# Kernel optimization log

Hardware: AMD Instinct MI355X
Metric: run time of the kernel (lower is better)

The kernel has to match this reference:

```python
import jax, jax.numpy as jnp
import numpy as np
import math

D, H = 128, 8
B, LC, LQ = 8, 512, 64


def pos_signal(channels, length):
    # tensor2tensor timing signal, returned as [C, L]
    pos = jnp.arange(length, dtype=jnp.float32)
    nts = channels // 2
    inc = math.log(1.0e4) / (nts - 1)
    inv = jnp.exp(jnp.arange(nts, dtype=jnp.float32) * -inc)
    st = pos[:, None] * inv[None, :]                      # [L, nts]
    sig = jnp.concatenate([jnp.sin(st), jnp.cos(st)], 1)  # [L, C]
    return sig.T


def mask_logits(t, m):
    return t * m + (1.0 - m) * -1e30


def ln_c(x, g, b):  # LayerNorm over channel dim of [B, D, L]
    mu = jnp.mean(x, axis=1, keepdims=True)
    var = jnp.mean((x - mu) ** 2, axis=1, keepdims=True)
    return (x - mu) / jnp.sqrt(var + 1e-5) * g[None, :, None] + b[None, :, None]


def conv1x1(x, w, b=None):  # x [B, I, L], w [O, I]
    y = jnp.einsum('oi,bil->bol', w, x)
    return y if b is None else y + b[None, :, None]


def dw_sep_conv(x, dw, pw, pwb):  # depthwise (k, no bias) -> pointwise (bias) -> relu
    k = dw.shape[-1]
    y = jax.lax.conv_general_dilated(x, dw[:, None, :], (1,), [(k // 2, k // 2)],
        dimension_numbers=('NCH', 'OIH', 'NCH'), feature_group_count=x.shape[1])
    return jax.nn.relu(conv1x1(y, pw, pwb))


def self_attention(x, mem_w, q_w, mask, n_head):  # x [B, D, L]
    b, d, L = x.shape
    dh = d // n_head
    mem = jnp.einsum('oi,bil->blo', mem_w, x)  # [B, L, 2D]
    q = jnp.einsum('oi,bil->blo', q_w, x)      # [B, L, D]
    def heads(t):
        return t.reshape(b, L, n_head, dh).transpose(0, 2, 1, 3)  # [B, H, L, dh]
    Qh = heads(q) * dh ** -0.5
    K = heads(mem[..., :d])
    V = heads(mem[..., d:])
    logits = jnp.einsum('bhqe,bhke->bhqk', Qh, K)
    logits = mask_logits(logits, mask[:, None, None, :])
    w = jax.nn.softmax(logits, axis=-1)
    o = jnp.einsum('bhqk,bhke->bhqe', w, V)
    return o.transpose(0, 2, 1, 3).reshape(b, L, d).transpose(0, 2, 1)


def encoder_block(x, mask, p, n_head):
    out = x + pos_signal(x.shape[1], x.shape[2])[None]
    n_conv = p['dw'].shape[0]
    for i in range(n_conv):
        res = out
        out = ln_c(out, p['lnc_g'][i], p['lnc_b'][i])
        out = dw_sep_conv(out, p['dw'][i], p['pw'][i], p['pw_b'][i]) + res
    res = out
    out = ln_c(out, p['ln1_g'], p['ln1_b'])
    out = self_attention(out, p['mem_w'], p['q_w'], mask, n_head) + res
    res = out
    out = ln_c(out, p['ln2_g'], p['ln2_b'])
    out = jax.nn.relu(conv1x1(out, p['ffn1_w'], p['ffn1_b']))
    out = conv1x1(out, p['ffn2_w'], p['ffn2_b'])
    return out + res


def cq_attention(Ce, Qe, cmask, qmask, w4C, w4Q, w4mlu, cq_b):
    Cx = Ce.transpose(0, 2, 1)   # [B, Lc, 2D]
    Qx = Qe.transpose(0, 2, 1)   # [B, Lq, 2D]
    s0 = jnp.einsum('bld,d->bl', Cx, w4C)[:, :, None]
    s1 = jnp.einsum('bqd,d->bq', Qx, w4Q)[:, None, :]
    s2 = jnp.einsum('bld,bqd->blq', Cx * w4mlu[None, None, :], Qx)
    S = s0 + s1 + s2 + cq_b
    S1 = jax.nn.softmax(mask_logits(S, qmask[:, None, :]), axis=2)
    S2 = jax.nn.softmax(mask_logits(S, cmask[:, :, None]), axis=1)
    A = jnp.einsum('blq,bqd->bld', S1, Qx)
    Bt = jnp.einsum('blq,bmq,bmd->bld', S1, S2, Cx)  # (S1 @ S2^T) @ C
    out = jnp.concatenate([Cx, A, Cx * A, Cx * Bt], axis=2)
    return out.transpose(0, 2, 1)  # [B, 8D, Lc]


def _forward(C, Q, maskC, maskQ, e_dw, e_pw, e_pw_b, e_lnc_g, e_lnc_b, e_mem_w, e_q_w,
             e_ffn1_w, e_ffn1_b, e_ffn2_w, e_ffn2_b, e_ln1_g, e_ln1_b, e_ln2_g, e_ln2_b,
             w4C, w4Q, w4mlu, cq_b, resizer_w,
             m_dw, m_pw, m_pw_b, m_lnc_g, m_lnc_b, m_mem_w, m_q_w,
             m_ffn1_w, m_ffn1_b, m_ffn2_w, m_ffn2_b, m_ln1_g, m_ln1_b, m_ln2_g, m_ln2_b):
    ep = dict(dw=e_dw, pw=e_pw, pw_b=e_pw_b, lnc_g=e_lnc_g, lnc_b=e_lnc_b,
              mem_w=e_mem_w, q_w=e_q_w, ffn1_w=e_ffn1_w, ffn1_b=e_ffn1_b,
              ffn2_w=e_ffn2_w, ffn2_b=e_ffn2_b, ln1_g=e_ln1_g, ln1_b=e_ln1_b,
              ln2_g=e_ln2_g, ln2_b=e_ln2_b)
    mp = dict(dw=m_dw, pw=m_pw, pw_b=m_pw_b, lnc_g=m_lnc_g, lnc_b=m_lnc_b,
              mem_w=m_mem_w, q_w=m_q_w, ffn1_w=m_ffn1_w, ffn1_b=m_ffn1_b,
              ffn2_w=m_ffn2_w, ffn2_b=m_ffn2_b, ln1_g=m_ln1_g, ln1_b=m_ln1_b,
              ln2_g=m_ln2_g, ln2_b=m_ln2_b)
    Ce = encoder_block(C, maskC, ep, H)
    Qe = encoder_block(Q, maskQ, ep, H)
    Ce = jnp.concatenate([Ce, C], axis=1)  # encode_fusion -> [B, 2D, Lc]
    Qe = jnp.concatenate([Qe, Q], axis=1)
    X = cq_attention(Ce, Qe, maskC, maskQ, w4C, w4Q, w4mlu, cq_b)
    X = jnp.concatenate([X, Ce], axis=1)   # match_fusion -> [B, 10D, Lc]
    M0 = conv1x1(X, resizer_w)             # [B, D, Lc]

    def run(m):
        def step(carry, p):
            return encoder_block(carry, maskC, p, H), None
        m, _ = jax.lax.scan(step, m, mp)
        return m

    M1 = run(M0)
    M2 = run(M1)
    M3 = run(M2)
    return M1, M2, M3


def setup_inputs() -> dict:
    key = jax.random.key(0)
    ks = iter(jax.random.split(key, 48))
    def rn(shape, scale):
        return jax.random.normal(next(ks), shape, dtype=jnp.float32) * scale
    s1 = 1.0 / math.sqrt(D)
    s2 = 1.0 / math.sqrt(2 * D)
    f32 = jnp.float32
    return dict(
        C=rn((B, D, LC), 1.0), Q=rn((B, D, LQ), 1.0),
        maskC=jnp.ones((B, LC), f32), maskQ=jnp.ones((B, LQ), f32),
        e_dw=rn((4, D, 7), 1.0 / math.sqrt(7)), e_pw=rn((4, D, D), s1),
        e_pw_b=jnp.zeros((4, D), f32), e_lnc_g=jnp.ones((4, D), f32), e_lnc_b=jnp.zeros((4, D), f32),
        e_mem_w=rn((2 * D, D), s1), e_q_w=rn((D, D), s1),
        e_ffn1_w=rn((D, D), s1), e_ffn1_b=jnp.zeros((D,), f32),
        e_ffn2_w=rn((D, D), s1), e_ffn2_b=jnp.zeros((D,), f32),
        e_ln1_g=jnp.ones((D,), f32), e_ln1_b=jnp.zeros((D,), f32),
        e_ln2_g=jnp.ones((D,), f32), e_ln2_b=jnp.zeros((D,), f32),
        w4C=rn((2 * D,), s2), w4Q=rn((2 * D,), s2), w4mlu=rn((2 * D,), s2),
        cq_b=jnp.zeros((1,), f32),
        resizer_w=rn((D, 10 * D), 1.0 / math.sqrt(10 * D)),
        m_dw=rn((7, 2, D, 5), 1.0 / math.sqrt(5)), m_pw=rn((7, 2, D, D), s1),
        m_pw_b=jnp.zeros((7, 2, D), f32), m_lnc_g=jnp.ones((7, 2, D), f32), m_lnc_b=jnp.zeros((7, 2, D), f32),
        m_mem_w=rn((7, 2 * D, D), s1), m_q_w=rn((7, D, D), s1),
        m_ffn1_w=rn((7, D, D), s1), m_ffn1_b=jnp.zeros((7, D), f32),
        m_ffn2_w=rn((7, D, D), s1), m_ffn2_b=jnp.zeros((7, D), f32),
        m_ln1_g=jnp.ones((7, D), f32), m_ln1_b=jnp.zeros((7, D), f32),
        m_ln2_g=jnp.ones((7, D), f32), m_ln2_b=jnp.zeros((7, D), f32),
    )


def reference(C, Q, maskC, maskQ, e_dw, e_pw, e_pw_b, e_lnc_g, e_lnc_b, e_mem_w, e_q_w,
              e_ffn1_w, e_ffn1_b, e_ffn2_w, e_ffn2_b, e_ln1_g, e_ln1_b, e_ln2_g, e_ln2_b,
              w4C, w4Q, w4mlu, cq_b, resizer_w,
              m_dw, m_pw, m_pw_b, m_lnc_g, m_lnc_b, m_mem_w, m_q_w,
              m_ffn1_w, m_ffn1_b, m_ffn2_w, m_ffn2_b, m_ln1_g, m_ln1_b, m_ln2_g, m_ln2_b):
    return _forward(C, Q, maskC, maskQ, e_dw, e_pw, e_pw_b, e_lnc_g, e_lnc_b, e_mem_w, e_q_w,
                    e_ffn1_w, e_ffn1_b, e_ffn2_w, e_ffn2_b, e_ln1_g, e_ln1_b, e_ln2_g, e_ln2_b,
                    w4C, w4Q, w4mlu, cq_b, resizer_w,
                    m_dw, m_pw, m_pw_b, m_lnc_g, m_lnc_b, m_mem_w, m_q_w,
                    m_ffn1_w, m_ffn1_b, m_ffn2_w, m_ffn2_b, m_ln1_g, m_ln1_b, m_ln2_g, m_ln2_b)
```

## Files before the change

kernel.cpp:

```cpp
#include <hip/hip_runtime.h>
#include <math.h>

#define D_  128
#define B_  8
#define H_  8
#define LC_ 512
#define LQ_ 64

typedef float f32x4 __attribute__((ext_vector_type(4)));
typedef short bf16x8 __attribute__((ext_vector_type(8)));
typedef short short4v __attribute__((ext_vector_type(4)));
typedef unsigned short ushortT;

__device__ inline short bfr(float x) {
  unsigned u = __float_as_uint(x);
  u += 0x7fff + ((u >> 16) & 1);
  return (short)(u >> 16);
}
__device__ inline float bfi(ushortT u) {
  return __uint_as_float(((unsigned)u) << 16);
}

__device__ inline bf16x8 mk8(short4v lo, short4v hi) {
  bf16x8 r;
  r[0] = lo[0]; r[1] = lo[1]; r[2] = lo[2]; r[3] = lo[3];
  r[4] = hi[0]; r[5] = hi[1]; r[6] = hi[2]; r[7] = hi[3];
  return r;
}

__device__ inline bf16x8 ldA(const ushortT* row, int koff) {
  short4v lo = *(const short4v*)(row + koff);
  short4v hi = *(const short4v*)(row + koff + 16);
  return mk8(lo, hi);
}
__device__ inline bf16x8 ldB2(const ushortT* plo, const ushortT* phi) {
  short4v lo = *(const short4v*)plo;
  short4v hi = *(const short4v*)phi;
  return mk8(lo, hi);
}

__global__ void k_prep(const float* a0, const float* a1, const float* a2,
                       const float* a3, const float* a4, const float* a5,
                       const float* a6, const float* a7, const float* a8,
                       const float* a9, const float* a10, ushortT* dst) {
  int i = blockIdx.x * 256 + threadIdx.x;
  if (i >= 1114112) return;
  const float* s; int lo;
  if      (i <   65536) { s = a0;  lo = i; }
  else if (i <   98304) { s = a1;  lo = i - 65536; }
  else if (i <  114688) { s = a2;  lo = i - 98304; }
  else if (i <  131072) { s = a3;  lo = i - 114688; }
  else if (i <  147456) { s = a4;  lo = i - 131072; }
  else if (i <  311296) { s = a5;  lo = i - 147456; }
  else if (i <  540672) { s = a6;  lo = i - 311296; }
  else if (i <  770048) { s = a7;  lo = i - 540672; }
  else if (i <  884736) { s = a8;  lo = i - 770048; }
  else if (i <  999424) { s = a9;  lo = i - 884736; }
  else                  { s = a10; lo = i - 999424; }
  dst[i] = (ushortT)bfr(s[lo]);
}

template <int KK, int ADDPOS>
__global__ __launch_bounds__(256) void k_fusedconv(
    const float* __restrict__ xC, float* __restrict__ yC,
    const float* __restrict__ xQ, float* __restrict__ yQ,
    const float* __restrict__ dw1, const ushortT* __restrict__ pw1,
    const float* __restrict__ pb1, const float* __restrict__ g1,
    const float* __restrict__ be1,
    const float* __restrict__ dw2, const ushortT* __restrict__ pw2,
    const float* __restrict__ pb2, const float* __restrict__ g2w,
    const float* __restrict__ be2, int ntC) {
  const int HALO = KK / 2;
  const int W1 = 32 + 2 * HALO;
  __shared__ __align__(16) float raw[128 * 40];
  __shared__ __align__(16) ushortT l1o[128 * 36];
  __shared__ __align__(16) ushortT xbf1[32 * 32 * 4];
  __shared__ float mu1[40], rs1[40], mu2[32], rs2[32], ps[160], psq[160];
  ushortT* xbf2 = (ushortT*)raw;
  int bx = blockIdx.x;
  const float* x; float* yout; int l0, L;
  if (bx < ntC) { x = xC; yout = yC; l0 = bx * 16; L = LC_; }
  else          { x = xQ; yout = yQ; l0 = (bx - ntC) * 16; L = LQ_; }
  int o0 = blockIdx.y * 64;
  int b = blockIdx.z;
  int tid = threadIdx.x;
  for (int idx = tid; idx < 128 * W1; idx += 256) {
    int d = idx / W1, c = idx - d * W1;
    int gl = l0 - 8 - HALO + c;
    float v = 0.f;
    if (gl >= 0 && gl < L) {
      v = x[((size_t)b * 128 + d) * L + gl];
      if (ADDPOS) {
        int j = d & 63;
        float arg = (float)gl * expf(-(float)j * 0.14619588f);
        v += (d < 64) ? sinf(arg) : cosf(arg);
      }
    }
    raw[d * 40 + c] = v;
  }
  __syncthreads();
  if (tid < 4 * W1) {
    int c = tid % W1, hh = tid / W1;
    float s = 0.f, s2 = 0.f;
    for (int d = hh * 32; d < hh * 32 + 32; d++) {
      float v = raw[d * 40 + c];
      s += v; s2 += v * v;
    }
    ps[tid] = s; psq[tid] = s2;
  }
  __syncthreads();
  if (tid < W1) {
    float s = ps[tid] + ps[tid + W1] + ps[tid + 2 * W1] + ps[tid + 3 * W1];
    float s2 = psq[tid] + psq[tid + W1] + psq[tid + 2 * W1] + psq[tid + 3 * W1];
    float mu = s * (1.f / 128.f);
    float var = fmaxf(s2 * (1.f / 128.f) - mu * mu, 0.f);
    mu1[tid] = mu; rs1[tid] = rsqrtf(var + 1e-5f);
  }
  __syncthreads();
  {
    int cc0 = tid & 31, dbase = tid >> 5;
#pragma unroll
    for (int kq = 0; kq < 4; kq++) {
      short4v pk;
#pragma unroll
      for (int e = 0; e < 4; e++) {
        int d = dbase * 16 + kq * 4 + e;
        float gg = g1[d], bb = be1[d];
        const float* wr = dw1 + d * KK;
        float acc = 0.f;
#pragma unroll
        for (int t = 0; t < KK; t++) {
          int ci = cc0 + t;
          int gl = l0 - 8 - HALO + ci;
          float lv = 0.f;
          if (gl >= 0 && gl < L)
            lv = (raw[d * 40 + ci] - mu1[ci]) * rs1[ci] * gg + bb;
          acc += wr[t] * lv;
        }
        pk[e] = bfr(acc);
      }
      *(short4v*)&xbf1[(((dbase * 4 + kq) * 32) + cc0) * 4] = pk;
    }
  }
  __syncthreads();
  int w = tid >> 6, lane = tid & 63, g2 = lane >> 4, r = lane & 15;
  {
    f32x4 acc[2][2];
#pragma unroll
    for (int i = 0; i < 2; i++)
// ... 43 lines not shown
    float s = ps[tid] + ps[tid + 32] + ps[tid + 64] + ps[tid + 96];
    float s2 = psq[tid] + psq[tid + 32] + psq[tid + 64] + psq[tid + 96];
    float mu = s * (1.f / 128.f);
    float var = fmaxf(s2 * (1.f / 128.f) - mu * mu, 0.f);
    mu2[tid] = mu; rs2[tid] = rsqrtf(var + 1e-5f);
  }
  __syncthreads();
  {
    int cc2 = tid & 15, db2 = tid >> 4;
#pragma unroll
    for (int kq = 0; kq < 2; kq++) {
      short4v pk;
#pragma unroll
      for (int e = 0; e < 4; e++) {
        int d = db2 * 8 + kq * 4 + e;
        float gg = g2w[d], bb = be2[d];
        const float* wr = dw2 + d * KK;
        float acc = 0.f;
#pragma unroll
        for (int t = 0; t < KK; t++) {
          int c1 = cc2 + 8 + t - HALO;
          int gl = l0 + cc2 + t - HALO;
          float lv = 0.f;
          if (gl >= 0 && gl < L)
            lv = (bfi(l1o[d * 36 + c1]) - mu2[c1]) * rs2[c1] * gg + bb;
          acc += wr[t] * lv;
        }
        pk[e] = bfr(acc);
      }
      *(short4v*)&xbf2[(((db2 * 2 + kq) * 16) + cc2) * 4] = pk;
    }
  }
  __syncthreads();
  {
    f32x4 a2 = {0.f, 0.f, 0.f, 0.f};
    const ushortT* arow = pw2 + (size_t)(o0 + 16 * w + r) * 128;
#pragma unroll
    for (int kk = 0; kk < 4; kk++) {
      bf16x8 a = ldA(arow, kk * 32 + g2 * 4);
      bf16x8 bb = ldB2(&xbf2[(((kk * 8 + g2) * 16) + r) * 4],
                       &xbf2[(((kk * 8 + 4 + g2) * 16) + r) * 4]);
      a2 = __builtin_amdgcn_mfma_f32_16x16x32_bf16(a, bb, a2, 0, 0, 0);
    }
#pragma unroll
    for (int p = 0; p < 4; p++) {
      int o = o0 + 16 * w + g2 * 4 + p;
      yout[((size_t)b * 128 + o) * L + l0 + r] =
          fmaxf(a2[p] + pb2[o], 0.f) + bfi(l1o[o * 36 + 8 + r]);
    }
  }
}

template <int KK, int ADDPOS>
__global__ __launch_bounds__(1024) void k_convproj1024(
    const float* __restrict__ xC, float* __restrict__ yC,
    float* __restrict__ mkvC, float* __restrict__ qpC,
    const float* __restrict__ xQ, float* __restrict__ yQ,
    float* __restrict__ mkvQ, float* __restrict__ qpQ,
    const float* __restrict__ dw1, const ushortT* __restrict__ pw1,
    const float* __restrict__ pb1, const float* __restrict__ g1,
    const float* __restrict__ be1,
    const float* __restrict__ dw2, const ushortT* __restrict__ pw2,
    const float* __restrict__ pb2, const float* __restrict__ g2w,
    const float* __restrict__ be2,
    const ushortT* __restrict__ memw, const ushortT* __restrict__ qw,
    const float* __restrict__ g3, const float* __restrict__ be3, int ntC) {
  const int HALO = KK / 2;
  const int W1 = 32 + 2 * HALO;
  __shared__ __align__(16) float raw[128 * 40];
  __shared__ __align__(16) ushortT l1o[128 * 36];
  __shared__ __align__(16) ushortT xbf1[32 * 32 * 4];
  __shared__ __align__(16) ushortT c2o[128 * 16];
  __shared__ float mu1[40], rs1[40], mu2[32], rs2[32], mu3[16], rs3[16];
  __shared__ float ps[160], psq[160];
  ushortT* xbf2 = (ushortT*)raw;
  ushortT* xbf3 = (ushortT*)(raw + 4096);
  int bx = blockIdx.x;
  const float* x; float* yout; float* mkv; float* qp; int l0, L;
  if (bx < ntC) { x = xC; yout = yC; mkv = mkvC; qp = qpC; l0 = bx * 16; L = LC_; }
  else          { x = xQ; yout = yQ; mkv = mkvQ; qp = qpQ; l0 = (bx - ntC) * 16; L = LQ_; }
  int b = blockIdx.z;
  int tid = threadIdx.x;
  for (int idx = tid; idx < 128 * W1; idx += 1024) {
    int d = idx / W1, c = idx - d * W1;
    int gl = l0 - 8 - HALO + c;
    float v = 0.f;
    if (gl >= 0 && gl < L) {
      v = x[((size_t)b * 128 + d) * L + gl];
      if (ADDPOS) {
        int j = d & 63;
        float arg = (float)gl * expf(-(float)j * 0.14619588f);
        v += (d < 64) ? sinf(arg) : cosf(arg);
      }
    }
    raw[d * 40 + c] = v;
  }
  __syncthreads();
  if (tid < 4 * W1) {
    int c = tid % W1, hh = tid / W1;
    float s = 0.f, s2 = 0.f;
    for (int d = hh * 32; d < hh * 32 + 32; d++) {
      float v = raw[d * 40 + c];
      s += v; s2 += v * v;
    }
    ps[tid] = s; psq[tid] = s2;
  }
  __syncthreads();
  if (tid < W1) {
    float s = ps[tid] + ps[tid + W1] + ps[tid + 2 * W1] + ps[tid + 3 * W1];
    float s2 = psq[tid] + psq[tid + W1] + psq[tid + 2 * W1] + psq[tid + 3 * W1];
    float mu = s * (1.f / 128.f);
    float var = fmaxf(s2 * (1.f / 128.f) - mu * mu, 0.f);
    mu1[tid] = mu; rs1[tid] = rsqrtf(var + 1e-5f);
  }
  __syncthreads();
  {
    int cc0 = tid & 31, dbase = tid >> 5;
    short4v pk;
#pragma unroll
    for (int e = 0; e < 4; e++) {
      int d = dbase * 4 + e;
      float gg = g1[d], bb = be1[d];
      const float* wr = dw1 + d * KK;
      float acc = 0.f;
#pragma unroll
      for (int t = 0; t < KK; t++) {
        int ci = cc0 + t;
        int gl = l0 - 8 - HALO + ci;
        float lv = 0.f;
        if (gl >= 0 && gl < L)
          lv = (raw[d * 40 + ci] - mu1[ci]) * rs1[ci] * gg + bb;
        acc += wr[t] * lv;
      }
      pk[e] = bfr(acc);
    }
    *(short4v*)&xbf1[((dbase * 32) + cc0) * 4] = pk;
  }
  __syncthreads();
  int w = tid >> 6, lane = tid & 63, g2 = lane >> 4, r = lane & 15;
  {
    int m = w & 7, nt = w >> 3;
    f32x4 acc = {0.f, 0.f, 0.f, 0.f};
    const ushortT* arow = pw1 + (size_t)(m * 16 + r) * 128;
#pragma unroll
    for (int kk = 0; kk < 4; kk++) {
      bf16x8 a = ldA(arow, kk * 32 + g2 * 4);
      bf16x8 bb = ldB2(&xbf1[(((kk * 8 + g2) * 32) + nt * 16 + r) * 4],
                       &xbf1[(((kk * 8 + 4 + g2) * 32) + nt * 16 + r) * 4]);
      acc = __builtin_amdgcn_mfma_f32_16x16x32_bf16(a, bb, acc, 0, 0, 0);
    }
#pragma unroll
    for (int p = 0; p < 4; p++) {
      int o = m * 16 + g2 * 4 + p;
      int c1 = nt * 16 + r;
      int gl = l0 - 8 + c1;
      float val = 0.f;
      if (gl >= 0 && gl < L)
        val = fmaxf(acc[p] + pb1[o], 0.f) + raw[o * 40 + c1 + HALO];
      l1o[o * 36 + c1] = (ushortT)bfr(val);
    }
  }
  __syncthreads();
  if (tid < 128) {
    int c = tid & 31, hh = tid >> 5;
    float s = 0.f, s2 = 0.f;
    for (int d = hh * 32; d < hh * 32 + 32; d++) {
      float v = bfi(l1o[d * 36 + c]);
      s += v; s2 += v * v;
    }
    ps[tid] = s; psq[tid] = s2;
  }
  __syncthreads();
  if (tid < 32) {
    float s = ps[tid] + ps[tid + 32] + ps[tid + 64] + ps[tid + 96];
    float s2 = psq[tid] + psq[tid + 32] + psq[tid + 64] + psq[tid + 96];
    float mu = s * (1.f / 128.f);
    float var = fmaxf(s2 * (1.f / 128.f) - mu * mu, 0.f);
    mu2[tid] = mu; rs2[tid] = rsqrtf(var + 1e-5f);
  }
  __syncthreads();
  {
    int cc2 = tid & 15, db2 = tid >> 4;
#pragma unroll
    for (int e = 0; e < 2; e++) {
      int d = db2 * 2 + e;
      float gg = g2w[d], bb = be2[d];
      const float* wr = dw2 + d * KK;
      float acc = 0.f;
#pragma unroll
      for (int t = 0; t < KK; t++) {
        int c1 = cc2 + 8 + t - HALO;
        int gl = l0 + cc2 + t - HALO;
        float lv = 0.f;
        if (gl >= 0 && gl < L)
          lv = (bfi(l1o[d * 36 + c1]) - mu2[c1]) * rs2[c1] * gg + bb;
        acc += wr[t] * lv;
      }
      xbf2[(((d >> 2) * 16) + cc2) * 4 + (d & 3)] = (ushortT)bfr(acc);
    }
  }
  __syncthreads();
  if (w < 8) {
    f32x4 a2 = {0.f, 0.f, 0.f, 0.f};
    const ushortT* arow = pw2 + (size_t)(w * 16 + r) * 128;
#pragma unroll
    for (int kk = 0; kk < 4; kk++) {
      bf16x8 a = ldA(arow, kk * 32 + g2 * 4);
      bf16x8 bb = ldB2(&xbf2[(((kk * 8 + g2) * 16) + r) * 4],
                       &xbf2[(((kk * 8 + 4 + g2) * 16) + r) * 4]);
      a2 = __builtin_amdgcn_mfma_f32_16x16x32_bf16(a, bb, a2, 0, 0, 0);
    }
#pragma unroll
    for (int p = 0; p < 4; p++) {
      int o = w * 16 + g2 * 4 + p;
      float val = fmaxf(a2[p] + pb2[o], 0.f) + bfi(l1o[o * 36 + 8 + r]);
      yout[((size_t)b * 128 + o) * L + l0 + r] = val;
      c2o[o * 16 + r] = (ushortT)bfr(val);
    }
  }
  __syncthreads();
  if (tid < 128) {
    int c = tid & 15, hh = tid >> 4;
    float s = 0.f, s2 = 0.f;
    for (int d = hh * 16; d < hh * 16 + 16; d++) {
      float v = bfi(c2o[d * 16 + c]);
      s += v; s2 += v * v;
    }
    ps[tid] = s; psq[tid] = s2;
  }
  __syncthreads();
  if (tid < 16) {
    float s = 0.f, s2 = 0.f;
#pragma unroll
    for (int hh = 0; hh < 8; hh++) { s += ps[hh * 16 + tid]; s2 += psq[hh * 16 + tid]; }
    float mu = s * (1.f / 128.f);
    float var = fmaxf(s2 * (1.f / 128.f) - mu * mu, 0.f);
    mu3[tid] = mu; rs3[tid] = rsqrtf(var + 1e-5f);
  }
  __syncthreads();
  for (int idx = tid; idx < 2048; idx += 1024) {
    int d = idx >> 4, c = idx & 15;
    float val = (bfi(c2o[d * 16 + c]) - mu3[c]) * rs3[c] * g3[d] + be3[d];
    xbf3[(((d >> 2) * 16) + c) * 4 + (d & 3)] = (ushortT)bfr(val);
  }
  __syncthreads();
#pragma unroll
  for (int t = 0; t < 2; t++) {
    int mt = w + 16 * t;
    if (mt < 24) {
      const ushortT* arow; float* outp; int obase, O;
      if (mt < 16) { arow = memw + (size_t)(mt * 16 + r) * 128; outp = mkv; obase = mt * 16; O = 256; }
      else         { arow = qw + (size_t)((mt - 16) * 16 + r) * 128; outp = qp; obase = (mt - 16) * 16; O = 128; }
      f32x4 acc = {0.f, 0.f, 0.f, 0.f};
#pragma unroll
      for (int kk = 0; kk < 4; kk++) {
        bf16x8 a = ldA(arow, kk * 32 + g2 * 4);
        bf16x8 bb = ldB2(&xbf3[(((kk * 8 + g2) * 16) + r) * 4],
                         &xbf3[(((kk * 8 + 4 + g2) * 16) + r) * 4]);
        acc = __builtin_amdgcn_mfma_f32_16x16x32_bf16(a, bb, acc, 0, 0, 0);
      }
#pragma unroll
      for (int p = 0; p < 4; p++)
        outp[((size_t)b * O + obase + g2 * 4 + p) * L + l0 + r] = acc[p];
    }
  }
}

template <int NCH, int WOUT>
__device__ __forceinline__ void attn_body(
    char* smem, const float* memKV, const float* qp, const float* mask,
    float* cur, const ushortT* w1bf, const float* b1,
    const ushortT* w2bf, const float* b2,
    const float* g, const float* be, float* wout, int q0, int b, int L, int tid) {
  float* msh = (float*)smem;
  float* ssh = (float*)(smem + 2048);
  float* OshF = (float*)(smem + 4096);
  float* updT = (float*)(smem + 12288);
  ushortT* xbf = (ushortT*)(smem + 20480);
  ushortT* midbf = (ushortT*)(smem + 24576);
  float* mu_s = (float*)(smem + 28672);
  float* rs_s = (float*)(smem + 28736);
  float* ps = (float*)(smem + 28800);
  float* psq = (float*)(smem + 32896);
  int w = tid >> 6;
  int h = w & 7, kh = w >> 3;
  int lane = tid & 63;
  int g2 = lane >> 4, r = lane & 15;
  const float* qb = qp + ((size_t)b * 128 + h * 16) * L;
  const float* kb = memKV + ((size_t)b * 256 + h * 16) * L;
  const float* vb = memKV + ((size_t)b * 256 + 128 + h * 16) * L;
  const float* mk = mask + (size_t)b * L;
  int qcol = q0 + r;
  bf16x8 qf;
#pragma unroll
  for (int j = 0; j < 4; j++)
    qf[j] = bfr(qb[(size_t)(g2 * 4 + j) * L + qcol] * 0.25f);
  qf[4] = 0; qf[5] = 0; qf[6] = 0; qf[7] = 0;
  float m_run = -INFINITY, ssum = 0.f;
  f32x4 O = {0.f, 0.f, 0.f, 0.f};
  int kbeg = kh * (L / 2), kend = (kh + 1) * (L / 2);
  for (int k0 = kbeg; k0 < kend; k0 += NCH * 16) {
    f32x4 sd[NCH];
#pragma unroll
    for (int mc = 0; mc < NCH; mc++) {
      bf16x8 kf;
      int krow = k0 + mc * 16 + r;
#pragma unroll
      for (int j = 0; j < 4; j++)
        kf[j] = bfr(kb[(size_t)(g2 * 4 + j) * L + krow]);
      kf[4] = 0; kf[5] = 0; kf[6] = 0; kf[7] = 0;
      f32x4 z = {0.f, 0.f, 0.f, 0.f};
      sd[mc] = __builtin_amdgcn_mfma_f32_16x16x32_bf16(kf, qf, z, 0, 0, 0);
    }
// ... 36 lines not shown
      float4 v0 = *(const float4*)vrow;
      float4 v1 = *(const float4*)(vrow + 16);
      bf16x8 vf;
      vf[0] = bfr(v0.x); vf[1] = bfr(v0.y); vf[2] = bfr(v0.z); vf[3] = bfr(v0.w);
      vf[4] = bfr(v1.x); vf[5] = bfr(v1.y); vf[6] = bfr(v1.z); vf[7] = bfr(v1.w);
      O = __builtin_amdgcn_mfma_f32_16x16x32_bf16(vf, pf[c2], O, 0, 0, 0);
    }
    m_run = nm;
  }
  if (kh == 1) {
    msh[h * 64 + lane] = m_run;
    ssh[h * 64 + lane] = ssum;
#pragma unroll
    for (int p = 0; p < 4; p++) OshF[(h * 64 + lane) * 4 + p] = O[p];
  }
  __syncthreads();
  if (kh == 0) {
    float mB = msh[h * 64 + lane], sB = ssh[h * 64 + lane];
    float nm = fmaxf(m_run, mB);
    float cA = __expf(m_run - nm), cB = __expf(mB - nm);
    float inv = 1.f / (ssum * cA + sB * cB);
#pragma unroll
    for (int p = 0; p < 4; p++) {
      int d = h * 16 + g2 * 4 + p;
      float ov = (O[p] * cA + OshF[(h * 64 + lane) * 4 + p] * cB) * inv;
      updT[d * 16 + r] = cur[((size_t)b * 128 + d) * L + qcol] + ov;
    }
  }
  __syncthreads();
  {
    int c = tid & 15, hh = tid >> 4;
    float s = 0.f, s2 = 0.f;
    for (int d = hh * 2; d < hh * 2 + 2; d++) {
      float v = updT[d * 16 + c];
      s += v; s2 += v * v;
    }
    ps[tid] = s; psq[tid] = s2;
  }
  __syncthreads();
  if (tid < 16) {
    float s = 0.f, s2 = 0.f;
    for (int hh = 0; hh < 64; hh++) { s += ps[hh * 16 + tid]; s2 += psq[hh * 16 + tid]; }
    float mu = s * (1.f / 128.f);
    float var = fmaxf(s2 * (1.f / 128.f) - mu * mu, 0.f);
    mu_s[tid] = mu; rs_s[tid] = rsqrtf(var + 1e-5f);
  }
  __syncthreads();
  for (int idx = tid; idx < 2048; idx += 1024) {
    int d = idx >> 4, c = idx & 15;
    float val = (updT[d * 16 + c] - mu_s[c]) * rs_s[c] * g[d] + be[d];
    xbf[(((d >> 2) * 16) + c) * 4 + (d & 3)] = (ushortT)bfr(val);
  }
  __syncthreads();
  if (w < 8) {
    f32x4 acc = {0.f, 0.f, 0.f, 0.f};
    const ushortT* ar = w1bf + (size_t)(16 * w + r) * 128;
#pragma unroll
    for (int kk = 0; kk < 4; kk++) {
      bf16x8 a = ldA(ar, kk * 32 + g2 * 4);
      bf16x8 bb = ldB2(&xbf[(((kk * 8 + g2) * 16) + r) * 4],
                       &xbf[(((kk * 8 + 4 + g2) * 16) + r) * 4]);
      acc = __builtin_amdgcn_mfma_f32_16x16x32_bf16(a, bb, acc, 0, 0, 0);
    }
#pragma unroll
    for (int p = 0; p < 4; p++) {
      int dmid = 16 * w + g2 * 4 + p;
      float val = fmaxf(acc[p] + b1[dmid], 0.f);
      midbf[(((4 * w + g2) * 16) + r) * 4 + p] = (ushortT)bfr(val);
    }
  }
  __syncthreads();
  if (w < 8) {
    f32x4 a2 = {0.f, 0.f, 0.f, 0.f};
    const ushortT* ar = w2bf + (size_t)(16 * w + r) * 128;
#pragma unroll
    for (int kk = 0; kk < 4; kk++) {
      bf16x8 a = ldA(ar, kk * 32 + g2 * 4);
      bf16x8 bb = ldB2(&midbf[(((kk * 8 + g2) * 16) + r) * 4],
                       &midbf[(((kk * 8 + 4 + g2) * 16) + r) * 4]);
      a2 = __builtin_amdgcn_mfma_f32_16x16x32_bf16(a, bb, a2, 0, 0, 0);
    }
#pragma unroll
    for (int p = 0; p < 4; p++) {
      int o = 16 * w + g2 * 4 + p;
      size_t pos = ((size_t)b * 128 + o) * L + q0 + r;
      float val = a2[p] + b2[o] + updT[o * 16 + r];
      cur[pos] = val;
      if (WOUT) wout[pos] = val;
    }
  }
}

template <int WOUT>
__global__ __launch_bounds__(1024) void k_attnffn_m(
    const float* memKV, const float* qp, const float* mask, float* cur,
    const ushortT* w1bf, const float* b1, const ushortT* w2bf, const float* b2,
    const float* g, const float* be, float* wout) {
  __shared__ __align__(16) char smem[36992];
  attn_body<8, WOUT>(smem, memKV, qp, mask, cur, w1bf, b1, w2bf, b2, g, be,
                     wout, blockIdx.x * 16, blockIdx.z, LC_, threadIdx.x);
}

__global__ __launch_bounds__(1024) void k_attnffn_in(
    const float* mkvC, const float* qpC, const float* maskC, float* curC,
    const float* mkvQ, const float* qpQ, const float* maskQ, float* curQ,
    const ushortT* w1bf, const float* b1, const ushortT* w2bf, const float* b2,
    const float* g, const float* be, int ntC) {
  __shared__ __align__(16) char smem[36992];
  int bx = blockIdx.x;
  if (bx < ntC)
    attn_body<8, 0>(smem, mkvC, qpC, maskC, curC, w1bf, b1, w2bf, b2, g, be,
                    nullptr, bx * 16, blockIdx.z, LC_, threadIdx.x);
  else
    attn_body<2, 0>(smem, mkvQ, qpQ, maskQ, curQ, w1bf, b1, w2bf, b2, g, be,
                    nullptr, (bx - ntC) * 16, blockIdx.z, LQ_, threadIdx.x);
}


__global__ void k_concat2m(const float* __restrict__ x1C, const float* __restrict__ x2C,
                           float* __restrict__ outC,
                           const float* __restrict__ x1Q, const float* __restrict__ x2Q,
                           float* __restrict__ outQ) {
  int idx = blockIdx.x * 256 + threadIdx.x;
  const int tot1 = B_ * 256 * LC_;
  const int tot2 = B_ * 256 * LQ_;
  if (idx < tot1) {
    int l = idx % LC_;
    int c = (idx / LC_) & 255;
    int b = idx / (LC_ * 256);
    float v = (c < 128) ? x1C[((size_t)b * 128 + c) * LC_ + l]
                        : x2C[((size_t)b * 128 + (c - 128)) * LC_ + l];
    outC[idx] = v;
  } else {
    int i2 = idx - tot1;
    if (i2 < tot2) {
      int l = i2 % LQ_;
      int c = (i2 / LQ_) & 255;
      int b = i2 / (LQ_ * 256);
      float v = (c < 128) ? x1Q[((size_t)b * 128 + c) * LQ_ + l]
                          : x2Q[((size_t)b * 128 + (c - 128)) * LQ_ + l];
      outQ[i2] = v;
// ... 174 lines not shown
  const float* w4C      = (const float*)d_in[19];
  const float* w4Q      = (const float*)d_in[20];
  const float* w4mlu    = (const float*)d_in[21];
  const float* cq_b     = (const float*)d_in[22];
  const float* resizer_w= (const float*)d_in[23];
  const float* m_dw     = (const float*)d_in[24];
  const float* m_pw     = (const float*)d_in[25];
  const float* m_pw_b   = (const float*)d_in[26];
  const float* m_lnc_g  = (const float*)d_in[27];
  const float* m_lnc_b  = (const float*)d_in[28];
  const float* m_mem_w  = (const float*)d_in[29];
  const float* m_q_w    = (const float*)d_in[30];
  const float* m_ffn1_w = (const float*)d_in[31];
  const float* m_ffn1_b = (const float*)d_in[32];
  const float* m_ffn2_w = (const float*)d_in[33];
  const float* m_ffn2_b = (const float*)d_in[34];
  const float* m_ln1_g  = (const float*)d_in[35];
  const float* m_ln1_b  = (const float*)d_in[36];
  const float* m_ln2_g  = (const float*)d_in[37];
  const float* m_ln2_b  = (const float*)d_in[38];

  float* ws = (float*)d_ws;
  const size_t SB = (size_t)B_ * D_ * LC_;
  float* cur  = ws;
  float* aux  = cur + SB;
  float* mkv  = aux + SB;
  float* qpb  = mkv + 2 * SB;
  float* Ce   = qpb + SB;
  float* Qe   = Ce + 2 * SB;
  float* Sbuf = Qe + (size_t)B_ * 256 * LQ_;
  float* S1   = Sbuf + (size_t)B_ * LC_ * LQ_;
  float* S2   = S1 + (size_t)B_ * LC_ * LQ_;
  float* Yb   = S2 + (size_t)B_ * LC_ * LQ_;
  float* Mb   = Yb + (size_t)B_ * 256 * LQ_;
  float* Ab   = mkv;
  float* Bb   = cur;
  ushortT* wb = (ushortT*)(Mb + SB);
  ushortT* w_epw  = wb;
  ushortT* w_emem = wb + 65536;
  ushortT* w_eq   = wb + 98304;
  ushortT* w_ef1  = wb + 114688;
  ushortT* w_ef2  = wb + 131072;
  ushortT* w_rsz  = wb + 147456;
  ushortT* w_mpw  = wb + 311296;
  ushortT* w_mmem = wb + 540672;
  ushortT* w_mq   = wb + 770048;
  ushortT* w_mf1  = wb + 884736;
  ushortT* w_mf2  = wb + 999424;
  float* after_wb = (float*)(wb + 1114112);
  float* curQ  = after_wb;
  float* auxQ  = curQ + 65536;
  float* mkvQ  = auxQ + 65536;
  float* qpbQ  = mkvQ + 131072;

  k_prep<<<(1114112 + 255) / 256, 256, 0, stream>>>(
      e_pw, e_mem_w, e_q_w, e_ffn1_w, e_ffn2_w, resizer_w,
      m_pw, m_mem_w, m_q_w, m_ffn1_w, m_ffn2_w, wb);

  k_fusedconv<7, 1><<<dim3(36, 2, B_), 256, 0, stream>>>(
      C, cur, Q, curQ,
      e_dw + 0 * 896, w_epw + 0, e_pw_b + 0, e_lnc_g + 0, e_lnc_b + 0,
      e_dw + 1 * 896, w_epw + 16384, e_pw_b + 128, e_lnc_g + 128, e_lnc_b + 128, 32);
  k_convproj1024<7, 0><<<dim3(36, 1, B_), 1024, 0, stream>>>(
      cur, aux, mkv, qpb, curQ, auxQ, mkvQ, qpbQ,
      e_dw + 2 * 896, w_epw + 32768, e_pw_b + 256, e_lnc_g + 256, e_lnc_b + 256,
      e_dw + 3 * 896, w_epw + 49152, e_pw_b + 384, e_lnc_g + 384, e_lnc_b + 384,
      w_emem, w_eq, e_ln1_g, e_ln1_b, 32);
  k_attnffn_in<<<dim3(36, 1, B_), 1024, 0, stream>>>(
      mkv, qpb, maskC, aux, mkvQ, qpbQ, maskQ, auxQ,
      w_ef1, e_ffn1_b, w_ef2, e_ffn2_b, e_ln2_g, e_ln2_b, 32);
  k_concat2m<<<(B_ * 256 * (LC_ + LQ_) + 255) / 256, 256, 0, stream>>>(
      aux, C, Ce, auxQ, Q, Qe);

  k_cqSrow<<<(B_ * LC_ * LQ_) / 256, 256, 0, stream>>>(Ce, Qe, w4C, w4Q, w4mlu, cq_b, maskQ, Sbuf, S1);
  k_softmax_col<<<B_ * LQ_, 256, 0, stream>>>(Sbuf, maskC, S2);
  k_cqY<<<(B_ * 256 * LQ_) / 256, 256, 0, stream>>>(S2, Ce, Yb);
  k_cqAB<<<dim3(LC_ / 64, 64, B_), 256, 0, stream>>>(S1, Qe, Yb, Ab, Bb);
  k_resizer512<<<dim3(LC_ / 16, 1, B_), 512, 0, stream>>>(Ce, Ab, Bb, w_rsz, Mb);

  float* out = (float*)d_out;
  float* bufs[2] = {cur, aux};
  int cb = 0;
  const float* src = Mb;
  for (int r = 0; r < 3; r++) {
    for (int bi = 0; bi < 7; bi++) {
      int pc0 = bi * 2, pc1 = bi * 2 + 1;
      float* ob = bufs[cb];
      k_convproj1024<5, 1><<<dim3(32, 1, B_), 1024, 0, stream>>>(
          src, ob, mkv, qpb, src, ob, mkv, qpb,
          m_dw + (size_t)pc0 * 640, w_mpw + (size_t)pc0 * 16384, m_pw_b + pc0 * 128,
          m_lnc_g + pc0 * 128, m_lnc_b + pc0 * 128,
          m_dw + (size_t)pc1 * 640, w_mpw + (size_t)pc1 * 16384, m_pw_b + pc1 * 128,
          m_lnc_g + pc1 * 128, m_lnc_b + pc1 * 128,
          w_mmem + (size_t)bi * 32768, w_mq + (size_t)bi * 16384,
          m_ln1_g + bi * 128, m_ln1_b + bi * 128, 32);
      if (bi == 6)
        k_attnffn_m<1><<<dim3(32, 1, B_), 1024, 0, stream>>>(
            mkv, qpb, maskC, ob,
            w_mf1 + (size_t)bi * 16384, m_ffn1_b + bi * 128,
            w_mf2 + (size_t)bi * 16384, m_ffn2_b + bi * 128,
            m_ln2_g + bi * 128, m_ln2_b + bi * 128, out + (size_t)r * SB);
      else
        k_attnffn_m<0><<<dim3(32, 1, B_), 1024, 0, stream>>>(
            mkv, qpb, maskC, ob,
            w_mf1 + (size_t)bi * 16384, m_ffn1_b + bi * 128,
            w_mf2 + (size_t)bi * 16384, m_ffn2_b + bi * 128,
            m_ln2_g + bi * 128, m_ln2_b + bi * 128, nullptr);
      src = ob;
      cb ^= 1;
    }
  }
}
```

Before: 1.335 ms.

## Halve conv-projection tile to 8 positions with 512 threads; precompute positional table

The fused two-conv plus projection kernel now handles 8 sequence positions per block with 512 threads instead of 16 with 1024. This doubles the grid, so more blocks can be spread across compute units and each block needs less shared memory. MFMA tiles become half-used, since only 8 of 16 columns are valid, and the halo overhead per block grows relative to the useful output. The sinusoidal position signal is also computed once into a table by a new kernel, so the conv kernels read it instead of calling expf/sinf/cosf in their load loops.

Measured after the change: 1.457 ms. +9.2%, slower.

```diff
diff --git a/kernel.cpp b/kernel.cpp
--- a/kernel.cpp
+++ b/kernel.cpp
@@ -60,10 +60,19 @@
   dst[i] = (ushortT)bfr(s[lo]);
 }
 
+__global__ void k_postab(float* pos) {
+  int i = blockIdx.x * 256 + threadIdx.x;
+  int d = i >> 9, l = i & 511;
+  int j = d & 63;
+  float arg = (float)l * expf(-(float)j * 0.14619588f);
+  pos[i] = (d < 64) ? sinf(arg) : cosf(arg);
+}
+
 template <int KK, int ADDPOS>
 __global__ __launch_bounds__(256) void k_fusedconv(
     const float* __restrict__ xC, float* __restrict__ yC,
     const float* __restrict__ xQ, float* __restrict__ yQ,
+    const float* __restrict__ pos,
     const float* __restrict__ dw1, const ushortT* __restrict__ pw1,
     const float* __restrict__ pb1, const float* __restrict__ g1,
     const float* __restrict__ be1,
@@ -90,11 +99,7 @@
     float v = 0.f;
     if (gl >= 0 && gl < L) {
       v = x[((size_t)b * 128 + d) * L + gl];
-      if (ADDPOS) {
-        int j = d & 63;
-        float arg = (float)gl * expf(-(float)j * 0.14619588f);
-        v += (d < 64) ? sinf(arg) : cosf(arg);
-      }
+      if (ADDPOS) v += pos[d * 512 + gl];
     }
     raw[d * 40 + c] = v;
   }
@@ -244,11 +249,12 @@
 }
 
 template <int KK, int ADDPOS>
-__global__ __launch_bounds__(1024) void k_convproj1024(
+__global__ __launch_bounds__(512) void k_convproj8(
     const float* __restrict__ xC, float* __restrict__ yC,
     float* __restrict__ mkvC, float* __restrict__ qpC,
     const float* __restrict__ xQ, float* __restrict__ yQ,
     float* __restrict__ mkvQ, float* __restrict__ qpQ,
+    const float* __restrict__ pos,
     const float* __restrict__ dw1, const ushortT* __restrict__ pw1,
     const float* __restrict__ pb1, const float* __restrict__ g1,
     const float* __restrict__ be1,
@@ -258,41 +264,37 @@
     const ushortT* __restrict__ memw, const ushortT* __restrict__ qw,
     const float* __restrict__ g3, const float* __restrict__ be3, int ntC) {
   const int HALO = KK / 2;
-  const int W1 = 32 + 2 * HALO;
-  __shared__ __align__(16) float raw[128 * 40];
-  __shared__ __align__(16) ushortT l1o[128 * 36];
-  __shared__ __align__(16) ushortT xbf1[32 * 32 * 4];
-  __shared__ __align__(16) ushortT c2o[128 * 16];
-  __shared__ float mu1[40], rs1[40], mu2[32], rs2[32], mu3[16], rs3[16];
-  __shared__ float ps[160], psq[160];
+  const int W1 = 16 + 2 * HALO;
+  __shared__ __align__(16) float raw[128 * 24];
+  __shared__ __align__(16) ushortT l1o[128 * 16];
+  __shared__ __align__(16) ushortT xbf1[128 * 16];
+  __shared__ __align__(16) ushortT c2o[128 * 8];
+  __shared__ float mu1[24], rs1[24], mu2[16], rs2[16], mu3[8], rs3[8];
+  __shared__ float ps[512], psq[512];
   ushortT* xbf2 = (ushortT*)raw;
-  ushortT* xbf3 = (ushortT*)(raw + 4096);
+  ushortT* xbf3 = (ushortT*)raw + 1024;
   int bx = blockIdx.x;
   const float* x; float* yout; float* mkv; float* qp; int l0, L;
-  if (bx < ntC) { x = xC; yout = yC; mkv = mkvC; qp = qpC; l0 = bx * 16; L = LC_; }
-  else          { x = xQ; yout = yQ; mkv = mkvQ; qp = qpQ; l0 = (bx - ntC) * 16; L = LQ_; }
+  if (bx < ntC) { x = xC; yout = yC; mkv = mkvC; qp = qpC; l0 = bx * 8; L = LC_; }
+  else          { x = xQ; yout = yQ; mkv = mkvQ; qp = qpQ; l0 = (bx - ntC) * 8; L = LQ_; }
   int b = blockIdx.z;
   int tid = threadIdx.x;
-  for (int idx = tid; idx < 128 * W1; idx += 1024) {
+  for (int idx = tid; idx < 128 * W1; idx += 512) {
     int d = idx / W1, c = idx - d * W1;
-    int gl = l0 - 8 - HALO + c;
+    int gl = l0 - 4 - HALO + c;
     float v = 0.f;
     if (gl >= 0 && gl < L) {
       v = x[((size_t)b * 128 + d) * L + gl];
-      if (ADDPOS) {
-        int j = d & 63;
-        float arg = (float)gl * expf(-(float)j * 0.14619588f);
-        v += (d < 64) ? sinf(arg) : cosf(arg);
-      }
-    }
-    raw[d * 40 + c] = v;
+      if (ADDPOS) v += pos[d * 512 + gl];
+    }
+    raw[d * 24 + c] = v;
   }
   __syncthreads();
   if (tid < 4 * W1) {
     int c = tid % W1, hh = tid / W1;
     float s = 0.f, s2 = 0.f;
     for (int d = hh * 32; d < hh * 32 + 32; d++) {
-      float v = raw[d * 40 + c];
+      float v = raw[d * 24 + c];
       s += v; s2 += v * v;
     }
     ps[tid] = s; psq[tid] = s2;
@@ -307,7 +309,7 @@
   }
   __syncthreads();
   {
-    int cc0 = tid & 31, dbase = tid >> 5;
+    int cc0 = tid & 15, dbase = tid >> 4;
     short4v pk;
 #pragma unroll
     for (int e = 0; e < 4; e++) {
@@ -318,61 +320,60 @@
 #pragma unroll
       for (int t = 0; t < KK; t++) {
         int ci = cc0 + t;
-        int gl = l0 - 8 - HALO + ci;
+        int gl = l0 - 4 - HALO + ci;
         float lv = 0.f;
         if (gl >= 0 && gl < L)
-          lv = (raw[d * 40 + ci] - mu1[ci]) * rs1[ci] * gg + bb;
+          lv = (raw[d * 24 + ci] - mu1[ci]) * rs1[ci] * gg + bb;
         acc += wr[t] * lv;
       }
       pk[e] = bfr(acc);
     }
-    *(short4v*)&xbf1[((dbase * 32) + cc0) * 4] = pk;
+    *(short4v*)&xbf1[((dbase * 16) + cc0) * 4] = pk;
   }
   __syncthreads();
   int w = tid >> 6, lane = tid & 63, g2 = lane >> 4, r = lane & 15;
   {
-    int m = w & 7, nt = w >> 3;
     f32x4 acc = {0.f, 0.f, 0.f, 0.f};
-    const ushortT* arow = pw1 + (size_t)(m * 16 + r) * 128;
+    const ushortT* arow = pw1 + (size_t)(w * 16 + r) * 128;
 #pragma unroll
     for (int kk = 0; kk < 4; kk++) {
       bf16x8 a = ldA(arow, kk * 32 + g2 * 4);
-      bf16x8 bb = ldB2(&xbf1[(((kk * 8 + g2) * 32) + nt * 16 + r) * 4],
-                       &xbf1[(((kk * 8 + 4 + g2) * 32) + nt * 16 + r) * 4]);
+      bf16x8 bb = ldB2(&xbf1[(((kk * 8 + g2) * 16) + r) * 4],
+                       &xbf1[(((kk * 8 + 4 + g2) * 16) + r) * 4]);
       acc = __builtin_amdgcn_mfma_f32_16x16x32_bf16(a, bb, acc, 0, 0, 0);
     }
 #pragma unroll
     for (int p = 0; p < 4; p++) {
-      int o = m * 16 + g2 * 4 + p;
-      int c1 = nt * 16 + r;
-      int gl = l0 - 8 + c1;
+      int o = w * 16 + g2 * 4 + p;
+      int gl = l0 - 4 + r;
       float val = 0.f;
       if (gl >= 0 && gl < L)
-        val = fmaxf(acc[p] + pb1[o], 0.f) + raw[o * 40 + c1 + HALO];
-      l1o[o * 36 + c1] = (ushortT)bfr(val);
-    }
-  }
-  __syncthreads();
-  if (tid < 128) {
-    int c = tid & 31, hh = tid >> 5;
+        val = fmaxf(acc[p] + pb1[o], 0.f) + raw[o * 24 + r + HALO];
+      l1o[o * 16 + r] = (ushortT)bfr(val);
+    }
+  }
+  __syncthreads();
+  {
+    int c = tid & 15, hh = tid >> 4;
     float s = 0.f, s2 = 0.f;
-    for (int d = hh * 32; d < hh * 32 + 32; d++) {
-      float v = bfi(l1o[d * 36 + c]);
+    for (int d = hh * 4; d < hh * 4 + 4; d++) {
+      float v = bfi(l1o[d * 16 + c]);
       s += v; s2 += v * v;
     }
     ps[tid] = s; psq[tid] = s2;
   }
   __syncthreads();
-  if (tid < 32) {
-    float s = ps[tid] + ps[tid + 32] + ps[tid + 64] + ps[tid + 96];
-    float s2 = psq[tid] + psq[tid + 32] + psq[tid + 64] + psq[tid + 96];
+  if (tid < 16) {
+    float s = 0.f, s2 = 0.f;
+#pragma unroll
+    for (int hh = 0; hh < 32; hh++) { s += ps[hh * 16 + tid]; s2 += psq[hh * 16 + tid]; }
     float mu = s * (1.f / 128.f);
     float var = fmaxf(s2 * (1.f / 128.f) - mu * mu, 0.f);
     mu2[tid] = mu; rs2[tid] = rsqrtf(var + 1e-5f);
   }
   __syncthreads();
   {
-    int cc2 = tid & 15, db2 = tid >> 4;
+    int cc2 = tid & 7, db2 = tid >> 3;
 #pragma unroll
     for (int e = 0; e < 2; e++) {
       int d = db2 * 2 + e;
@@ -381,76 +382,78 @@
       float acc = 0.f;
 #pragma unroll
       for (int t = 0; t < KK; t++) {
-        int c1 = cc2 + 8 + t - HALO;
+        int c1 = cc2 + 4 + t - HALO;
         int gl = l0 + cc2 + t - HALO;
         float lv = 0.f;
         if (gl >= 0 && gl < L)
-          lv = (bfi(l1o[d * 36 + c1]) - mu2[c1]) * rs2[c1] * gg + bb;
+          lv = (bfi(l1o[d * 16 + c1]) - mu2[c1]) * rs2[c1] * gg + bb;
         acc += wr[t] * lv;
       }
-      xbf2[(((d >> 2) * 16) + cc2) * 4 + (d & 3)] = (ushortT)bfr(acc);
-    }
-  }
-  __syncthreads();
-  if (w < 8) {
+      xbf2[(((d >> 2) * 8) + cc2) * 4 + (d & 3)] = (ushortT)bfr(acc);
+    }
+  }
+  __syncthreads();
+  {
     f32x4 a2 = {0.f, 0.f, 0.f, 0.f};
     const ushortT* arow = pw2 + (size_t)(w * 16 + r) * 128;
 #pragma unroll
     for (int kk = 0; kk < 4; kk++) {
       bf16x8 a = ldA(arow, kk * 32 + g2 * 4);
-      bf16x8 bb = ldB2(&xbf2[(((kk * 8 + g2) * 16) + r) * 4],
-                       &xbf2[(((kk * 8 + 4 + g2) * 16) + r) * 4]);
+      bf16x8 bb = ldB2(&xbf2[(((kk * 8 + g2) * 8) + (r & 7)) * 4],
+                       &xbf2[(((kk * 8 + 4 + g2) * 8) + (r & 7)) * 4]);
       a2 = __builtin_amdgcn_mfma_f32_16x16x32_bf16(a, bb, a2, 0, 0, 0);
     }
-#pragma unroll
-    for (int p = 0; p < 4; p++) {
-      int o = w * 16 + g2 * 4 + p;
-      float val = fmaxf(a2[p] + pb2[o], 0.f) + bfi(l1o[o * 36 + 8 + r]);
-      yout[((size_t)b * 128 + o) * L + l0 + r] = val;
-      c2o[o * 16 + r] = (ushortT)bfr(val);
-    }
-  }
-  __syncthreads();
-  if (tid < 128) {
-    int c = tid & 15, hh = tid >> 4;
+    if (r < 8) {
+#pragma unroll
+      for (int p = 0; p < 4; p++) {
+        int o = w * 16 + g2 * 4 + p;
+        float val = fmaxf(a2[p] + pb2[o], 0.f) + bfi(l1o[o * 16 + 4 + r]);
+        yout[((size_t)b * 128 + o) * L + l0 + r] = val;
+        c2o[o * 8 + r] = (ushortT)bfr(val);
+      }
+    }
+  }
+  __syncthreads();
+  {
+    int c = tid & 7, hh = tid >> 3;
     float s = 0.f, s2 = 0.f;
-    for (int d = hh * 16; d < hh * 16 + 16; d++) {
-      float v = bfi(c2o[d * 16 + c]);
+    for (int d = hh * 2; d < hh * 2 + 2; d++) {
+      float v = bfi(c2o[d * 8 + c]);
       s += v; s2 += v * v;
     }
     ps[tid] = s; psq[tid] = s2;
   }
   __syncthreads();
-  if (tid < 16) {
+  if (tid < 8) {
     float s = 0.f, s2 = 0.f;
 #pragma unroll
-    for (int hh = 0; hh < 8; hh++) { s += ps[hh * 16 + tid]; s2 += psq[hh * 16 + tid]; }
+    for (int hh = 0; hh < 64; hh++) { s += ps[hh * 8 + tid]; s2 += psq[hh * 8 + tid]; }
     float mu = s * (1.f / 128.f);
     float var = fmaxf(s2 * (1.f / 128.f) - mu * mu, 0.f);
     mu3[tid] = mu; rs3[tid] = rsqrtf(var + 1e-5f);
   }
   __syncthreads();
-  for (int idx = tid; idx < 2048; idx += 1024) {
-    int d = idx >> 4, c = idx & 15;
-    float val = (bfi(c2o[d * 16 + c]) - mu3[c]) * rs3[c] * g3[d] + be3[d];
-    xbf3[(((d >> 2) * 16) + c) * 4 + (d & 3)] = (ushortT)bfr(val);
-  }
-  __syncthreads();
-#pragma unroll
-  for (int t = 0; t < 2; t++) {
-    int mt = w + 16 * t;
-    if (mt < 24) {
-      const ushortT* arow; float* outp; int obase, O;
-      if (mt < 16) { arow = memw + (size_t)(mt * 16 + r) * 128; outp = mkv; obase = mt * 16; O = 256; }
-      else         { arow = qw + (size_t)((mt - 16) * 16 + r) * 128; outp = qp; obase = (mt - 16) * 16; O = 128; }
-      f32x4 acc = {0.f, 0.f, 0.f, 0.f};
-#pragma unroll
-      for (int kk = 0; kk < 4; kk++) {
-        bf16x8 a = ldA(arow, kk * 32 + g2 * 4);
-        bf16x8 bb = ldB2(&xbf3[(((kk * 8 + g2) * 16) + r) * 4],
-                         &xbf3[(((kk * 8 + 4 + g2) * 16) + r) * 4]);
-        acc = __builtin_amdgcn_mfma_f32_16x16x32_bf16(a, bb, acc, 0, 0, 0);
-      }
+  for (int idx = tid; idx < 1024; idx += 512) {
+    int d = idx >> 3, c = idx & 7;
+    float val = (bfi(c2o[d * 8 + c]) - mu3[c]) * rs3[c] * g3[d] + be3[d];
+    xbf3[(((d >> 2) * 8) + c) * 4 + (d & 3)] = (ushortT)bfr(val);
+  }
+  __syncthreads();
+#pragma unroll
+  for (int t = 0; t < 3; t++) {
+    int mt = w + 8 * t;
+    const ushortT* arow; float* outp; int obase, O;
+    if (mt < 16) { arow = memw + (size_t)(mt * 16 + r) * 128; outp = mkv; obase = mt * 16; O = 256; }
+    else         { arow = qw + (size_t)((mt - 16) * 16 + r) * 128; outp = qp; obase = (mt - 16) * 16; O = 128; }
+    f32x4 acc = {0.f, 0.f, 0.f, 0.f};
+#pragma unroll
+    for (int kk = 0; kk < 4; kk++) {
+      bf16x8 a = ldA(arow, kk * 32 + g2 * 4);
+      bf16x8 bb = ldB2(&xbf3[(((kk * 8 + g2) * 8) + (r & 7)) * 4],
+                       &xbf3[(((kk * 8 + 4 + g2) * 8) + (r & 7)) * 4]);
+      acc = __builtin_amdgcn_mfma_f32_16x16x32_bf16(a, bb, acc, 0, 0, 0);
+    }
+    if (r < 8) {
 #pragma unroll
       for (int p = 0; p < 4; p++)
         outp[((size_t)b * O + obase + g2 * 4 + p) * L + l0 + r] = acc[p];
@@ -593,41 +596,43 @@
     xbf[(((d >> 2) * 16) + c) * 4 + (d & 3)] = (ushortT)bfr(val);
   }
   __syncthreads();
-  if (w < 8) {
+  int w8 = tid >> 6;
+  int g2b = (tid & 63) >> 4, rb = tid & 15;
+  if (w8 < 8) {
     f32x4 acc = {0.f, 0.f, 0.f, 0.f};
-    const ushortT* ar = w1bf + (size_t)(16 * w + r) * 128;
+    const ushortT* ar = w1bf + (size_t)(16 * w8 + rb) * 128;
 #pragma unroll
     for (int kk = 0; kk < 4; kk++) {
-      bf16x8 a = ldA(ar, kk * 32 + g2 * 4);
-      bf16x8 bb = ldB2(&xbf[(((kk * 8 + g2) * 16) + r) * 4],
-                       &xbf[(((kk * 8 + 4 + g2) * 16) + r) * 4]);
+      bf16x8 a = ldA(ar, kk * 32 + g2b * 4);
+      bf16x8 bb = ldB2(&xbf[(((kk * 8 + g2b) * 16) + rb) * 4],
+                       &xbf[(((kk * 8 + 4 + g2b) * 16) + rb) * 4]);
       acc = __builtin_amdgcn_mfma_f32_16x16x32_bf16(a, bb, acc, 0, 0, 0);
     }
 #pragma unroll
     for (int p = 0; p < 4; p++) {
-      int dmid = 16 * w + g2 * 4 + p;
+      int dmid = 16 * w8 + g2b * 4 + p;
       float val = fmaxf(acc[p] + b1[dmid], 0.f);
-      midbf[(((4 * w + g2) * 16) + r) * 4 + p] = (ushortT)bfr(val);
-    }
-  }
-  __syncthreads();
-  if (w < 8) {
+      midbf[(((4 * w8 + g2b) * 16) + rb) * 4 + p] = (ushortT)bfr(val);
+    }
+  }
+  __syncthreads();
+  if (w8 < 8) {
     f32x4 a2 = {0.f, 0.f, 0.f, 0.f};
-    const ushortT* ar = w2bf + (size_t)(16 * w + r) * 128;
+    const ushortT* ar = w2bf + (size_t)(16 * w8 + rb) * 128;
 #pragma unroll
     for (int kk = 0; kk < 4; kk++) {
-      bf16x8 a = ldA(ar, kk * 32 + g2 * 4);
-      bf16x8 bb = ldB2(&midbf[(((kk * 8 + g2) * 16) + r) * 4],
-                       &midbf[(((kk * 8 + 4 + g2) * 16) + r) * 4]);
+      bf16x8 a = ldA(ar, kk * 32 + g2b * 4);
+      bf16x8 bb = ldB2(&midbf[(((kk * 8 + g2b) * 16) + rb) * 4],
+                       &midbf[(((kk * 8 + 4 + g2b) * 16) + rb) * 4]);
       a2 = __builtin_amdgcn_mfma_f32_16x16x32_bf16(a, bb, a2, 0, 0, 0);
     }
 #pragma unroll
     for (int p = 0; p < 4; p++) {
-      int o = 16 * w + g2 * 4 + p;
-      size_t pos = ((size_t)b * 128 + o) * L + q0 + r;
-      float val = a2[p] + b2[o] + updT[o * 16 + r];
-      cur[pos] = val;
-      if (WOUT) wout[pos] = val;
+      int o = 16 * w8 + g2b * 4 + p;
+      size_t pos2 = ((size_t)b * 128 + o) * L + q0 + rb;
+      float val = a2[p] + b2[o] + updT[o * 16 + rb];
+      cur[pos2] = val;
+      if (WOUT) wout[pos2] = val;
     }
   }
 }
@@ -908,20 +913,22 @@
   float* auxQ  = curQ + 65536;
   float* mkvQ  = auxQ + 65536;
   float* qpbQ  = mkvQ + 131072;
+  float* posT  = qpbQ + 65536;
 
   k_prep<<<(1114112 + 255) / 256, 256, 0, stream>>>(
       e_pw, e_mem_w, e_q_w, e_ffn1_w, e_ffn2_w, resizer_w,
       m_pw, m_mem_w, m_q_w, m_ffn1_w, m_ffn2_w, wb);
+  k_postab<<<256, 256, 0, stream>>>(posT);
 
   k_fusedconv<7, 1><<<dim3(36, 2, B_), 256, 0, stream>>>(
-      C, cur, Q, curQ,
+      C, cur, Q, curQ, posT,
       e_dw + 0 * 896, w_epw + 0, e_pw_b + 0, e_lnc_g + 0, e_lnc_b + 0,
       e_dw + 1 * 896, w_epw + 16384, e_pw_b + 128, e_lnc_g + 128, e_lnc_b + 128, 32);
-  k_convproj1024<7, 0><<<dim3(36, 1, B_), 1024, 0, stream>>>(
-      cur, aux, mkv, qpb, curQ, auxQ, mkvQ, qpbQ,
+  k_convproj8<7, 0><<<dim3(72, 1, B_), 512, 0, stream>>>(
+      cur, aux, mkv, qpb, curQ, auxQ, mkvQ, qpbQ, posT,
       e_dw + 2 * 896, w_epw + 32768, e_pw_b + 256, e_lnc_g + 256, e_lnc_b + 256,
       e_dw + 3 * 896, w_epw + 49152, e_pw_b + 384, e_lnc_g + 384, e_lnc_b + 384,
-      w_emem, w_eq, e_ln1_g, e_ln1_b, 32);
+      w_emem, w_eq, e_ln1_g, e_ln1_b, 64);
   k_attnffn_in<<<dim3(36, 1, B_), 1024, 0, stream>>>(
       mkv, qpb, maskC, aux, mkvQ, qpbQ, maskQ, auxQ,
       w_ef1, e_ffn1_b, w_ef2, e_ffn2_b, e_ln2_g, e_ln2_b, 32);
@@ -942,14 +949,14 @@
     for (int bi = 0; bi < 7; bi++) {
       int pc0 = bi * 2, pc1 = bi * 2 + 1;
       float* ob = bufs[cb];
-      k_convproj1024<5, 1><<<dim3(32, 1, B_), 1024, 0, stream>>>(
-          src, ob, mkv, qpb, src, ob, mkv, qpb,
+      k_convproj8<5, 1><<<dim3(64, 1, B_), 512, 0, stream>>>(
+          src, ob, mkv, qpb, src, ob, mkv, qpb, posT,
           m_dw + (size_t)pc0 * 640, w_mpw + (size_t)pc0 * 16384, m_pw_b + pc0 * 128,
           m_lnc_g + pc0 * 128, m_lnc_b + pc0 * 128,
           m_dw + (size_t)pc1 * 640, w_mpw + (size_t)pc1 * 16384, m_pw_b + pc1 * 128,
           m_lnc_g + pc1 * 128, m_lnc_b + pc1 * 128,
           w_mmem + (size_t)bi * 32768, w_mq + (size_t)bi * 16384,
-          m_ln1_g + bi * 128, m_ln1_b + bi * 128, 32);
+          m_ln1_g + bi * 128, m_ln1_b + bi * 128, 64);
       if (bi == 6)
         k_attnffn_m<1><<<dim3(32, 1, B_), 1024, 0, stream>>>(
             mkv, qpb, maskC, ob,
```
